# Optimization experiments

Measured on AMD Instinct MI355X. Metric: run time of the kernel, lower is better.

## Reference

```python
import jax, jax.numpy as jnp
import numpy as np

NUM_HEADS = 16
ROPE_BASE = 10000.0


def _rope(q, k, seq_len, head_dim):
    # cos/sin: [S, D] -> broadcast over batch and heads via [:, None, :]
    inv_freq = 1.0 / (ROPE_BASE ** (jnp.arange(0, head_dim, 2, dtype=jnp.float32) / head_dim))
    t = jnp.arange(seq_len, dtype=jnp.float32)
    freqs = t[:, None] * inv_freq[None, :]            # [S, D/2]
    emb = jnp.concatenate((freqs, freqs), axis=-1)    # [S, D]
    cos = jnp.cos(emb)[:, None, :]                    # [S, 1, D]
    sin = jnp.sin(emb)[:, None, :]
    def rot(x):
        return jnp.stack([-x[..., 1::2], x[..., ::2]], axis=-1).reshape(x.shape)
    q = q * cos + rot(q) * sin
    k = k * cos + rot(k) * sin
    return q, k


def setup_inputs() -> dict:
    key = jax.random.key(0)
    ks = jax.random.split(key, 5)
    B, S, D = 2, 2048, 2048
    return {
        "hidden_states": jax.random.normal(ks[0], (B, S, D), dtype=jnp.float32),
        "Wq": jax.random.normal(ks[1], (D, D), dtype=jnp.float32) * 0.02,
        "Wk": jax.random.normal(ks[2], (D, D), dtype=jnp.float32) * 0.02,
        "Wv": jax.random.normal(ks[3], (D, D), dtype=jnp.float32) * 0.02,
        "Wo": jax.random.normal(ks[4], (D, D), dtype=jnp.float32) * 0.02,
        "attention_mask": jnp.ones((B, S), dtype=bool),
        "position_ids": S,  # passed to rotary as seq_len
    }


def reference(hidden_states, Wq, Wk, Wv, Wo, attention_mask, position_ids):
    B, S, D = hidden_states.shape
    H = NUM_HEADS
    hd = D // H
    q = (hidden_states @ Wq.T).reshape(B, S, H, hd)
    k = (hidden_states @ Wk.T).reshape(B, S, H, hd)
    v = (hidden_states @ Wv.T).reshape(B, S, H, hd)
    q, k = _rope(q, k, position_ids, hd)
    scores = jnp.einsum('bqhd,bkhd->bhqk', q, k) / jnp.sqrt(jnp.float32(hd))
    scores = jnp.where(attention_mask[:, None, None, :], scores, -jnp.inf)
    attn = jax.nn.softmax(scores, axis=-1)
    out = jnp.einsum('bhqk,bkhd->bqhd', attn, v).reshape(B, S, D)
    return out @ Wo.T
```

## Files before the change

kernel.cpp:

```cpp
#include <hip/hip_runtime.h>
#include <hip/hip_bf16.h>
#include <math.h>

typedef __hip_bfloat16 bf16;
typedef __attribute__((ext_vector_type(8))) short bf16x8;
typedef __attribute__((ext_vector_type(4))) float f32x4;

#define AS1 __attribute__((address_space(1)))
#define AS3 __attribute__((address_space(3)))

static constexpr int BATCH = 2, S = 2048, D = 2048, H = 16, HD = 128;
static constexpr int M = BATCH * S;
static constexpr float SCALE = 0.08838834764831845f;

__device__ __forceinline__ void gload_lds16(const void* g, void* l) {
  __builtin_amdgcn_global_load_lds((AS1 void*)g, (AS3 void*)l, 16, 0, 0);
}

__device__ __forceinline__ unsigned short f2bu(float f) {
  bf16 h = __float2bfloat16(f);
  return *reinterpret_cast<unsigned short*>(&h);
}

__global__ void cast_kernel(const float* __restrict__ in,
                            unsigned short* __restrict__ out, int n4) {
  int i = blockIdx.x * blockDim.x + threadIdx.x;
  int stride = gridDim.x * blockDim.x;
  for (; i < n4; i += stride) {
    float4 v = reinterpret_cast<const float4*>(in)[i];
    ushort4 o;
    o.x = f2bu(v.x); o.y = f2bu(v.y); o.z = f2bu(v.z); o.w = f2bu(v.w);
    reinterpret_cast<ushort4*>(out)[i] = o;
  }
}

__global__ void rope_tab_kernel(float2* __restrict__ cs) {
  int s = blockIdx.x, j = threadIdx.x;
  double inv = exp(-(double)j * 0.14391156831212793);
  float ang = (float)s * (float)inv;
  double da = (double)ang;
  cs[s * 64 + j] = make_float2((float)cos(da), (float)sin(da));
}

template <int EPI>
__global__ __launch_bounds__(256, 2) void gemm_bt(const bf16* __restrict__ A,
                                                  const bf16* __restrict__ B,
                                                  void* __restrict__ outp,
                                                  const float2* __restrict__ cs) {
  constexpr int K = 2048;
  __shared__ bf16 smA[2][128 * 32];
  __shared__ bf16 smB[2][128 * 32];
  const int tid = threadIdx.x;
  const int l = tid & 63, w = tid >> 6;
  const int wm = w >> 1, wn = w & 1;
  const int bm = blockIdx.y, bn = blockIdx.x;
  const int lr = l & 15, lg = l >> 4;

  f32x4 acc[4][4] = {};

  auto stage = [&](bf16* dst, const bf16* src, int row0, int k0) {
    #pragma unroll
    for (int i = 0; i < 2; ++i) {
      int idx = tid + i * 256;
      int row = idx >> 2, seg = idx & 3;
      gload_lds16(src + (size_t)(row0 + row) * K + k0 + seg * 8, dst + idx * 8);
    }
  };

  stage(smA[0], A, bm * 128, 0);
  stage(smB[0], B, bn * 128, 0);
  asm volatile("s_waitcnt vmcnt(0)" ::: "memory");
  __syncthreads();

  for (int kt = 0; kt < K / 32; ++kt) {
    const int cur = kt & 1;
    if (kt + 1 < K / 32) {
      stage(smA[cur ^ 1], A, bm * 128, (kt + 1) * 32);
      stage(smB[cur ^ 1], B, bn * 128, (kt + 1) * 32);
    }
    bf16x8 af[4], bfr[4];
    #pragma unroll
    for (int fm = 0; fm < 4; ++fm)
      af[fm] = *reinterpret_cast<const bf16x8*>(
          &smA[cur][(wm * 64 + fm * 16 + lr) * 32 + lg * 8]);
    #pragma unroll
    for (int fn = 0; fn < 4; ++fn)
      bfr[fn] = *reinterpret_cast<const bf16x8*>(
          &smB[cur][(wn * 64 + fn * 16 + lr) * 32 + lg * 8]);
    #pragma unroll
    for (int fm = 0; fm < 4; ++fm)
      #pragma unroll
      for (int fn = 0; fn < 4; ++fn)
        acc[fm][fn] = __builtin_amdgcn_mfma_f32_16x16x32_bf16(af[fm], bfr[fn],
                                                              acc[fm][fn], 0, 0, 0);
    __syncthreads();
  }

  const int row0 = bm * 128 + wm * 64 + lg * 4;
  const int col0 = bn * 128 + wn * 64 + lr;

  if constexpr (EPI == 0) {
    bf16* o = reinterpret_cast<bf16*>(outp);
    #pragma unroll
    for (int fm = 0; fm < 4; ++fm) {
      #pragma unroll
      for (int fn = 0; fn < 4; ++fn) {
        const int col = col0 + fn * 16;
        const int j = col & 63;
        const bool odd = (col & 1);
        #pragma unroll
        for (int r = 0; r < 4; ++r) {
          float v = acc[fm][fn][r];
          float p = __shfl_xor(v, 1);
          int row = row0 + fm * 16 + r;
          int s = row & (S - 1);
          float2 c = cs[s * 64 + j];
          float nv = v * c.x + (odd ? p : -p) * c.y;
          o[(size_t)row * D + col] = __float2bfloat16(nv);
        }
      }
    }
  } else if constexpr (EPI == 1) {
    bf16* o = reinterpret_cast<bf16*>(outp);
    #pragma unroll
    for (int fm = 0; fm < 4; ++fm) {
      #pragma unroll
      for (int fn = 0; fn < 4; ++fn) {
        int row = row0 + fm * 16;
        int col = col0 + fn * 16;
        int b_ = row >> 11, sp = row & (S - 1);
        int h = col >> 7, d = col & (HD - 1);
        size_t off = ((size_t)(b_ * H + h) * HD + d) * S + sp;
        ushort4 pk;
        pk.x = f2bu(acc[fm][fn][0]);
        pk.y = f2bu(acc[fm][fn][1]);
        pk.z = f2bu(acc[fm][fn][2]);
        pk.w = f2bu(acc[fm][fn][3]);
        *reinterpret_cast<ushort4*>(o + off) = pk;
      }
    }
  } else {
    float* o = reinterpret_cast<float*>(outp);
    #pragma unroll
    for (int fm = 0; fm < 4; ++fm)
      #pragma unroll
      for (int fn = 0; fn < 4; ++fn)
        #pragma unroll
        for (int r = 0; r < 4; ++r)
          o[(size_t)(row0 + fm * 16 + r) * D + col0 + fn * 16] = acc[fm][fn][r];
  }
}

__global__ __launch_bounds__(256, 2) void attn_kernel(const bf16* __restrict__ Q,
                                                      const bf16* __restrict__ Kmat,
                                                      const bf16* __restrict__ Vt,
                                                      bf16* __restrict__ O) {
  __shared__ bf16 kv_lds[2][16384];
  __shared__ bf16 plds[4][16][72];
  const int tid = threadIdx.x;
  const int l = tid & 63, w = tid >> 6;
  const int lr = l & 15, lg = l >> 4;
  const int bh = blockIdx.y;
  const int b = bh >> 4, h = bh & 15;
  const int q0 = blockIdx.x * 64 + w * 16;

  bf16x8 aq[4];
  #pragma unroll
  for (int ks = 0; ks < 4; ++ks)
    aq[ks] = *reinterpret_cast<const bf16x8*>(
        &Q[((size_t)b * S + q0 + lr) * D + h * HD + ks * 32 + lg * 8]);

  const bf16* ksrc[4];
  const bf16* vsrc[4];
  int kldsoff[4], vldsoff[4];
  #pragma unroll
  for (int i = 0; i < 4; ++i) {
    int idx = tid + i * 256;
    int krow = idx >> 4, kcb = (idx & 15) << 4;
    int kcol = (kcb ^ ((krow & 7) << 4)) >> 1;
    ksrc[i] = Kmat + ((size_t)b * S + krow) * D + h * HD + kcol;
    kldsoff[i] = idx * 8;
    int vrow = idx >> 3, vcb = (idx & 7) << 4;
    int vcol = (vcb ^ ((vrow & 7) << 4)) >> 1;
    vsrc[i] = Vt + ((size_t)bh * HD + vrow) * S + vcol;
    vldsoff[i] = 8192 + idx * 8;
  }

  auto stage = [&](int buf, int t) {
    #pragma unroll
    for (int i = 0; i < 4; ++i) {
      gload_lds16(ksrc[i] + (size_t)t * 64 * D, &kv_lds[buf][kldsoff[i]]);
      gload_lds16(vsrc[i] + t * 64, &kv_lds[buf][vldsoff[i]]);
    }
  };

  f32x4 oacc[8] = {};
  float m[4], ls[4];
  #pragma unroll
  for (int r = 0; r < 4; ++r) { m[r] = -1e30f; ls[r] = 0.f; }

  stage(0, 0);
  asm volatile("s_waitcnt vmcnt(0)" ::: "memory");
  __syncthreads();

  const int swz = (lr & 7) << 4;

  for (int t = 0; t < S / 64; ++t) {
    const int cur = t & 1;
    if (t + 1 < S / 64) stage(cur ^ 1, t + 1);
    const bf16* Kl = &kv_lds[cur][0];
    const bf16* Vl = &kv_lds[cur][8192];

    f32x4 sf[4] = {};
    #pragma unroll
    for (int ksub = 0; ksub < 4; ++ksub) {
      #pragma unroll
      for (int ks = 0; ks < 4; ++ks) {
        bf16x8 bk = *reinterpret_cast<const bf16x8*>(
            &Kl[(ksub * 16 + lr) * 128 + (((ks * 64 + lg * 16) ^ swz) >> 1)]);
        sf[ksub] = __builtin_amdgcn_mfma_f32_16x16x32_bf16(aq[ks], bk, sf[ksub], 0, 0, 0);
      }
    }
    #pragma unroll
    for (int r = 0; r < 4; ++r) {
      float mx = fmaxf(fmaxf(sf[0][r], sf[1][r]), fmaxf(sf[2][r], sf[3][r]));
      #pragma unroll
      for (int off = 1; off < 16; off <<= 1) mx = fmaxf(mx, __shfl_xor(mx, off));
      float mn = fmaxf(m[r], mx * SCALE);
      float al = __expf(m[r] - mn);
      m[r] = mn;
      ls[r] *= al;
      #pragma unroll
      for (int df = 0; df < 8; ++df) oacc[df][r] *= al;
      float psum = 0.f;
      #pragma unroll
      for (int ksub = 0; ksub < 4; ++ksub) {
        float p = __expf(sf[ksub][r] * SCALE - mn);
        psum += p;
        plds[w][lg * 4 + r][ksub * 16 + lr] = __float2bfloat16(p);
      }
      #pragma unroll
      for (int off = 1; off < 16; off <<= 1) psum += __shfl_xor(psum, off);
      ls[r] += psum;
    }
    bf16x8 pa0 = *reinterpret_cast<const bf16x8*>(&plds[w][lr][lg * 8]);
    bf16x8 pa1 = *reinterpret_cast<const bf16x8*>(&plds[w][lr][32 + lg * 8]);
    #pragma unroll
    for (int df = 0; df < 8; ++df) {
      const int vr = df * 16 + lr;
      bf16x8 bv0 = *reinterpret_cast<const bf16x8*>(
          &Vl[vr * 64 + (((lg * 16) ^ swz) >> 1)]);
      bf16x8 bv1 = *reinterpret_cast<const bf16x8*>(
          &Vl[vr * 64 + (((64 + lg * 16) ^ swz) >> 1)]);
      oacc[df] = __builtin_amdgcn_mfma_f32_16x16x32_bf16(pa0, bv0, oacc[df], 0, 0, 0);
      oacc[df] = __builtin_amdgcn_mfma_f32_16x16x32_bf16(pa1, bv1, oacc[df], 0, 0, 0);
    }
    asm volatile("s_waitcnt vmcnt(0)" ::: "memory");
    __syncthreads();
  }
  #pragma unroll
  for (int df = 0; df < 8; ++df) {
    #pragma unroll
    for (int r = 0; r < 4; ++r) {
      float v = oacc[df][r] / ls[r];
      O[((size_t)b * S + q0 + lg * 4 + r) * D + h * HD + df * 16 + lr] =
          __float2bfloat16(v);
    }
  }
}

extern "C" void kernel_launch(void* const* d_in, const int* in_sizes, int n_in,
                              void* d_out, int out_size, void* d_ws, size_t ws_size,
                              hipStream_t stream) {
  const float* hs = (const float*)d_in[0];
  const float* Wq = (const float*)d_in[1];
  const float* Wk = (const float*)d_in[2];
  const float* Wv = (const float*)d_in[3];
  const float* Wo = (const float*)d_in[4];
  float* out = (float*)d_out;

  const size_t nTok = (size_t)M * D;
  const size_t nW = (size_t)D * D;
  bf16* hsb = (bf16*)d_ws;
  bf16* wqb = hsb + nTok;
  bf16* wkb = wqb + nW;
  bf16* wvb = wkb + nW;
  bf16* wob = wvb + nW;
  bf16* qb  = wob + nW;
  bf16* kb  = qb + nTok;
  bf16* vtb = kb + nTok;
  bf16* ob  = vtb + nTok;
  float2* cs = (float2*)(ob + nTok);

  cast_kernel<<<2048, 256, 0, stream>>>(hs, (unsigned short*)hsb, (int)(nTok / 4));
  cast_kernel<<<1024, 256, 0, stream>>>(Wq, (unsigned short*)wqb, (int)(nW / 4));
  cast_kernel<<<1024, 256, 0, stream>>>(Wk, (unsigned short*)wkb, (int)(nW / 4));
  cast_kernel<<<1024, 256, 0, stream>>>(Wv, (unsigned short*)wvb, (int)(nW / 4));
  cast_kernel<<<1024, 256, 0, stream>>>(Wo, (unsigned short*)wob, (int)(nW / 4));
  rope_tab_kernel<<<S, 64, 0, stream>>>(cs);

  dim3 gg(D / 128, M / 128);
  gemm_bt<0><<<gg, 256, 0, stream>>>(hsb, wqb, qb, cs);
  gemm_bt<0><<<gg, 256, 0, stream>>>(hsb, wkb, kb, cs);
  gemm_bt<1><<<gg, 256, 0, stream>>>(hsb, wvb, vtb, nullptr);

  attn_kernel<<<dim3(S / 64, BATCH * H), 256, 0, stream>>>(qb, kb, vtb, ob);

  gemm_bt<2><<<gg, 256, 0, stream>>>(ob, wob, out, nullptr);
}
```

Before: 515.5 us.

## Fold softmax scale into Q, lazy rescale, defer row-sum reduction, add MFMA priority

The attention scale is folded into the Q projection epilogue, so the inner loop no longer multiplies scores by SCALE. The online-softmax max update and accumulator rescale are skipped when no lane's max grows by more than 8 (an FA4-style lazy rescale). Per-row sums now stay per lane and are shuffle-reduced once at the end, with a reciprocal multiply replacing the division. s_setprio hints are placed around the MFMA blocks. Skipping the rescale lets p values exceed 1 by up to e^8, which adds some bf16 rounding risk but stays within range.

```diff
diff --git a/kernel.cpp b/kernel.cpp
--- a/kernel.cpp
+++ b/kernel.cpp
@@ -46,7 +46,8 @@
 __global__ __launch_bounds__(256, 2) void gemm_bt(const bf16* __restrict__ A,
                                                   const bf16* __restrict__ B,
                                                   void* __restrict__ outp,
-                                                  const float2* __restrict__ cs) {
+                                                  const float2* __restrict__ cs,
+                                                  float oscale) {
   constexpr int K = 2048;
   __shared__ bf16 smA[2][128 * 32];
   __shared__ bf16 smB[2][128 * 32];
@@ -115,7 +116,7 @@
           int row = row0 + fm * 16 + r;
           int s = row & (S - 1);
           float2 c = cs[s * 64 + j];
-          float nv = v * c.x + (odd ? p : -p) * c.y;
+          float nv = (v * c.x + (odd ? p : -p) * c.y) * oscale;
           o[(size_t)row * D + col] = __float2bfloat16(nv);
         }
       }
@@ -212,6 +213,7 @@
     const bf16* Vl = &kv_lds[cur][8192];
 
     f32x4 sf[4] = {};
+    __builtin_amdgcn_s_setprio(1);
     #pragma unroll
     for (int ksub = 0; ksub < 4; ++ksub) {
       #pragma unroll
@@ -221,30 +223,32 @@
         sf[ksub] = __builtin_amdgcn_mfma_f32_16x16x32_bf16(aq[ks], bk, sf[ksub], 0, 0, 0);
       }
     }
+    __builtin_amdgcn_s_setprio(0);
+
     #pragma unroll
     for (int r = 0; r < 4; ++r) {
       float mx = fmaxf(fmaxf(sf[0][r], sf[1][r]), fmaxf(sf[2][r], sf[3][r]));
       #pragma unroll
       for (int off = 1; off < 16; off <<= 1) mx = fmaxf(mx, __shfl_xor(mx, off));
-      float mn = fmaxf(m[r], mx * SCALE);
-      float al = __expf(m[r] - mn);
-      m[r] = mn;
-      ls[r] *= al;
-      #pragma unroll
-      for (int df = 0; df < 8; ++df) oacc[df][r] *= al;
-      float psum = 0.f;
+      if (!__all(mx <= m[r] + 8.f)) {
+        float mn = fmaxf(m[r], mx);
+        float al = __expf(m[r] - mn);
+        m[r] = mn;
+        ls[r] *= al;
+        #pragma unroll
+        for (int df = 0; df < 8; ++df) oacc[df][r] *= al;
+      }
       #pragma unroll
       for (int ksub = 0; ksub < 4; ++ksub) {
-        float p = __expf(sf[ksub][r] * SCALE - mn);
-        psum += p;
+        float p = __expf(sf[ksub][r] - m[r]);
+        ls[r] += p;
         plds[w][lg * 4 + r][ksub * 16 + lr] = __float2bfloat16(p);
       }
-      #pragma unroll
-      for (int off = 1; off < 16; off <<= 1) psum += __shfl_xor(psum, off);
-      ls[r] += psum;
-    }
+    }
+
     bf16x8 pa0 = *reinterpret_cast<const bf16x8*>(&plds[w][lr][lg * 8]);
     bf16x8 pa1 = *reinterpret_cast<const bf16x8*>(&plds[w][lr][32 + lg * 8]);
+    __builtin_amdgcn_s_setprio(1);
     #pragma unroll
     for (int df = 0; df < 8; ++df) {
       const int vr = df * 16 + lr;
@@ -255,14 +259,22 @@
       oacc[df] = __builtin_amdgcn_mfma_f32_16x16x32_bf16(pa0, bv0, oacc[df], 0, 0, 0);
       oacc[df] = __builtin_amdgcn_mfma_f32_16x16x32_bf16(pa1, bv1, oacc[df], 0, 0, 0);
     }
+    __builtin_amdgcn_s_setprio(0);
     asm volatile("s_waitcnt vmcnt(0)" ::: "memory");
     __syncthreads();
   }
+
+  #pragma unroll
+  for (int r = 0; r < 4; ++r) {
+    #pragma unroll
+    for (int off = 1; off < 16; off <<= 1) ls[r] += __shfl_xor(ls[r], off);
+    ls[r] = 1.0f / ls[r];
+  }
   #pragma unroll
   for (int df = 0; df < 8; ++df) {
     #pragma unroll
     for (int r = 0; r < 4; ++r) {
-      float v = oacc[df][r] / ls[r];
+      float v = oacc[df][r] * ls[r];
       O[((size_t)b * S + q0 + lg * 4 + r) * D + h * HD + df * 16 + lr] =
           __float2bfloat16(v);
     }
@@ -300,11 +312,11 @@
   rope_tab_kernel<<<S, 64, 0, stream>>>(cs);
 
   dim3 gg(D / 128, M / 128);
-  gemm_bt<0><<<gg, 256, 0, stream>>>(hsb, wqb, qb, cs);
-  gemm_bt<0><<<gg, 256, 0, stream>>>(hsb, wkb, kb, cs);
-  gemm_bt<1><<<gg, 256, 0, stream>>>(hsb, wvb, vtb, nullptr);
+  gemm_bt<0><<<gg, 256, 0, stream>>>(hsb, wqb, qb, cs, SCALE);
+  gemm_bt<0><<<gg, 256, 0, stream>>>(hsb, wkb, kb, cs, 1.0f);
+  gemm_bt<1><<<gg, 256, 0, stream>>>(hsb, wvb, vtb, nullptr, 1.0f);
 
   attn_kernel<<<dim3(S / 64, BATCH * H), 256, 0, stream>>>(qb, kb, vtb, ob);
 
-  gemm_bt<2><<<gg, 256, 0, stream>>>(ob, wob, out, nullptr);
-}
+  gemm_bt<2><<<gg, 256, 0, stream>>>(ob, wob, out, nullptr, 1.0f);
+}
```

Result: faster. 499.4 us (-3.1%).
